# Kernel optimization log

Measured on AMD Instinct MI355X. Metric: run time of the kernel, lower is better.

The kernel has to match this reference:

```python
import jax, jax.numpy as jnp
import numpy as np

B, L, IN_DIMS = 256, 512, 64
UNITS, OUT_STEPS, OUT_DIMS = 256, 64, 32
KSIZE = 5


def setup_inputs() -> dict:
    key = jax.random.key(0)
    ks = jax.random.split(key, 14)
    s = lambda k, shp: jax.random.normal(k, shp, dtype=jnp.float32) * 0.05
    return {
        "inputs": jax.random.normal(ks[0], (B, L, IN_DIMS), dtype=jnp.float32),
        "conv_k": s(ks[1], (KSIZE, IN_DIMS, UNITS)),   # WIO layout
        "conv_b": s(ks[2], (UNITS,)),
        "enc_W": s(ks[3], (UNITS, 4 * UNITS)),          # kernel (input after CNN has UNITS channels)
        "enc_U": s(ks[4], (UNITS, 4 * UNITS)),          # recurrent kernel
        "enc_b": s(ks[5], (4 * UNITS,)),
        "cell_W": s(ks[6], (UNITS, 4 * UNITS)),
        "cell_U": s(ks[7], (UNITS, 4 * UNITS)),
        "cell_b": s(ks[8], (4 * UNITS,)),
        "fore_W": s(ks[9], (UNITS, OUT_DIMS)),
        "fore_b": s(ks[10], (OUT_DIMS,)),
        "back_W": s(ks[11], (UNITS, IN_DIMS)),
        "back_b": s(ks[12], (IN_DIMS,)),
    }


def _lstm_step(W, U, b, h, c, x_t):
    # Keras gate order: i, f, g(candidate), o
    z = x_t @ W + h @ U + b
    i, f, g, o = jnp.split(z, 4, axis=-1)
    c_new = jax.nn.sigmoid(f) * c + jax.nn.sigmoid(i) * jnp.tanh(g)
    h_new = jax.nn.sigmoid(o) * jnp.tanh(c_new)
    return h_new, c_new


def _forward(inputs, conv_k, conv_b, enc_W, enc_U, enc_b,
             cell_W, cell_U, cell_b, fore_W, fore_b, back_W, back_b):
    # Conv1D 'same', relu
    x = jax.lax.conv_general_dilated(
        inputs, conv_k, window_strides=(1,), padding="SAME",
        dimension_numbers=("NWC", "WIO", "NWC"))
    x = jax.nn.relu(x + conv_b)

    # Encoder LSTM (dropout inactive at inference)
    h0 = jnp.zeros((x.shape[0], UNITS), x.dtype)
    c0 = jnp.zeros((x.shape[0], UNITS), x.dtype)

    def enc_step(carry, x_t):
        h, c = carry
        h, c = _lstm_step(enc_W, enc_U, enc_b, h, c, x_t)
        return (h, c), h
    (h_T, c_T), seq = jax.lax.scan(enc_step, (h0, c0), jnp.swapaxes(x, 0, 1))
    backcast_seq = jnp.swapaxes(seq, 0, 1)  # [B, L, UNITS]

    def dec_step(carry, _):
        h, c = carry
        h, c = _lstm_step(cell_W, cell_U, cell_b, h, c, h)
        return (h, c), h
    _, outs = jax.lax.scan(dec_step, (h_T, c_T), None, length=OUT_STEPS)
    forecast_seq = jnp.swapaxes(outs, 0, 1)  # [B, OUT_STEPS, UNITS]

    forecast = forecast_seq @ fore_W + fore_b   # [B, OUT_STEPS, OUT_DIMS]
    backcast = backcast_seq @ back_W + back_b   # [B, L, IN_DIMS]
    return forecast, backcast


def reference(inputs, conv_k, conv_b, enc_W, enc_U, enc_b,
              cell_W, cell_U, cell_b, fore_W, fore_b, back_W, back_b):
    return _forward(inputs, conv_k, conv_b, enc_W, enc_U, enc_b,
                    cell_W, cell_U, cell_b, fore_W, fore_b, back_W, back_b)
```

## Files before the change

kernel.cpp:

```cpp
#include <hip/hip_runtime.h>
#include <stdint.h>

typedef unsigned short u16;
typedef __attribute__((ext_vector_type(8))) short bf16x8;
typedef __attribute__((ext_vector_type(4))) float fx4;

#define MFMA16(a, b, c) __builtin_amdgcn_mfma_f32_16x16x32_bf16((a), (b), (c), 0, 0, 0)

#define OFF_X      0u
#define OFF_H      67108864u
#define OFF_ENCWT  142737408u
#define OFF_ENCUT  143261696u
#define OFF_CELLT  143785984u
#define OFF_CONVKT 144310272u
#define OFF_BWT    144474112u
#define OFF_FWT    144506880u
#define OFF_BAR    144523264u

__device__ __forceinline__ u16 f2bf(float f) {
    uint32_t u = __builtin_bit_cast(uint32_t, f);
    u += 0x7FFFu + ((u >> 16) & 1u);
    return (u16)(u >> 16);
}
__device__ __forceinline__ float sigm(float x) { return 1.0f / (1.0f + __expf(-x)); }
__device__ __forceinline__ float tanh_f(float x) { return 1.0f - 2.0f / (__expf(2.0f * x) + 1.0f); }

__device__ __forceinline__ void store_h_sc(const u16* p, uint32_t v) {
    asm volatile("global_store_short %0, %1, off sc0 sc1" :: "v"(p), "v"(v) : "memory");
}
__device__ __forceinline__ void vmcnt0() { asm volatile("s_waitcnt vmcnt(0)" ::: "memory"); }

__global__ void zero_kernel(unsigned char* ws) {
    int i = blockIdx.x * blockDim.x + threadIdx.x;
    uint32_t* h0 = (uint32_t*)(ws + OFF_H);
    for (int k = i; k < 32768; k += 16384) h0[k] = 0u;
    if (i < 256) ((uint32_t*)(ws + OFF_BAR))[i] = 0u;
}

__global__ void prep_kernel(const float* enc_W, const float* enc_U, const float* cell_W,
                            const float* cell_U, const float* conv_k, const float* back_W,
                            const float* fore_W, unsigned char* ws) {
    u16* encWt = (u16*)(ws + OFF_ENCWT);
    u16* encUt = (u16*)(ws + OFF_ENCUT);
    u16* cellT = (u16*)(ws + OFF_CELLT);
    u16* convKt = (u16*)(ws + OFF_CONVKT);
    u16* bwt = (u16*)(ws + OFF_BWT);
    u16* fwt = (u16*)(ws + OFF_FWT);
    int idx = blockIdx.x * blockDim.x + threadIdx.x;
    int stride = gridDim.x * blockDim.x;
    for (int i = idx; i < 262144; i += stride) {
        int n = i >> 8, k = i & 255;
        encWt[i] = f2bf(enc_W[k * 1024 + n]);
        encUt[i] = f2bf(enc_U[k * 1024 + n]);
        cellT[i] = f2bf(cell_W[k * 1024 + n] + cell_U[k * 1024 + n]);
    }
    for (int i = idx; i < 81920; i += stride) {
        int u = i / 320, rem = i - u * 320;
        convKt[i] = f2bf(conv_k[rem * 256 + u]);
    }
    for (int i = idx; i < 16384; i += stride) {
        int n = i >> 8, k = i & 255;
        bwt[i] = f2bf(back_W[k * 64 + n]);
    }
    for (int i = idx; i < 8192; i += stride) {
        int n = i >> 8, k = i & 255;
        fwt[i] = f2bf(fore_W[k * 32 + n]);
    }
}

__global__ __launch_bounds__(256) void conv_kernel(const float* __restrict__ in,
                                                   const float* __restrict__ conv_b,
                                                   unsigned char* ws) {
    const u16* kt = (const u16*)(ws + OFF_CONVKT);
    u16* xout = (u16*)(ws + OFF_X);
    int w = threadIdx.x >> 6, lane = threadIdx.x & 63;
    int m = lane & 15, q = lane >> 4;
    int mt = blockIdx.x * 4 + w;
    int r0 = mt * 16;
    int b = r0 >> 9;
    int l0 = r0 & 511;

    fx4 acc[16];
#pragma unroll
    for (int nt = 0; nt < 16; ++nt) acc[nt] = (fx4){0.f, 0.f, 0.f, 0.f};

#pragma unroll
    for (int s = 0; s < 10; ++s) {
        int k0 = s * 32 + q * 8;
        int kk = k0 >> 6, c = k0 & 63;
        int l2 = l0 + m + kk - 2;
        bf16x8 af = {0, 0, 0, 0, 0, 0, 0, 0};
        if (l2 >= 0 && l2 < 512) {
            const float* src = in + (((b << 9) + l2) << 6) + c;
            fx4 f0 = *(const fx4*)src;
            fx4 f1 = *(const fx4*)(src + 4);
            af[0] = (short)f2bf(f0[0]); af[1] = (short)f2bf(f0[1]);
            af[2] = (short)f2bf(f0[2]); af[3] = (short)f2bf(f0[3]);
            af[4] = (short)f2bf(f1[0]); af[5] = (short)f2bf(f1[1]);
            af[6] = (short)f2bf(f1[2]); af[7] = (short)f2bf(f1[3]);
        }
#pragma unroll
        for (int nt = 0; nt < 16; ++nt) {
            bf16x8 bf = *(const bf16x8*)(kt + (nt * 16 + m) * 320 + k0);
            acc[nt] = MFMA16(af, bf, acc[nt]);
        }
    }
#pragma unroll
    for (int nt = 0; nt < 16; ++nt) {
        int u = nt * 16 + m;
        float bias = conv_b[u];
#pragma unroll
        for (int r = 0; r < 4; ++r) {
            float v = acc[nt][r] + bias;
            v = v > 0.f ? v : 0.f;
            int row = r0 + q * 4 + r;
            xout[row * 256 + u] = f2bf(v);
        }
    }
}

__global__ __launch_bounds__(256, 1) void enc_kernel(const float* __restrict__ enc_b,
                                                     unsigned char* ws) {
    int tid = threadIdx.x;
    int w = tid >> 6, lane = tid & 63, m = lane & 15, q = lane >> 4;
    int bid = blockIdx.x;
    int g = bid & 15, p = bid >> 4;
    int b0 = g * 16;
    int un0 = p * 64 + w * 16;

    const u16* encWt = (const u16*)(ws + OFF_ENCWT);
    const u16* encUt = (const u16*)(ws + OFF_ENCUT);
    const u16* xbf = (const u16*)(ws + OFF_X);
    u16* H = (u16*)(ws + OFF_H);
    float* csaveg = (float*)(ws + OFF_X + (size_t)g * 4194304u);
    int* bar = (int*)(ws + OFF_BAR + g * 64);

    bf16x8 wfrag[4][8], ufrag[4][8];
#pragma unroll
    for (int gi = 0; gi < 4; ++gi) {
#pragma unroll
        for (int s = 0; s < 8; ++s) {
            int n = gi * 256 + un0 + m;
            wfrag[gi][s] = *(const bf16x8*)(encWt + n * 256 + s * 32 + q * 8);
            ufrag[gi][s] = *(const bf16x8*)(encUt + n * 256 + s * 32 + q * 8);
        }
    }
    float bi[4], creg[4];
#pragma unroll
    for (int gi = 0; gi < 4; ++gi) bi[gi] = enc_b[gi * 256 + un0 + m];
    creg[0] = creg[1] = creg[2] = creg[3] = 0.f;

    const u16* xrow = xbf + (size_t)(b0 + m) * (512 * 256) + q * 8;

    for (int t = 0; t < 512; ++t) {
        bf16x8 xa[8];
        const u16* xA = xrow + (size_t)t * 256;
#pragma unroll
        for (int s = 0; s < 8; ++s) xa[s] = *(const bf16x8*)(xA + s * 32);
        fx4 acc[4];
#pragma unroll
        for (int gi = 0; gi < 4; ++gi) acc[gi] = (fx4){bi[gi], bi[gi], bi[gi], bi[gi]};
#pragma unroll
        for (int s = 0; s < 8; ++s) {
#pragma unroll
            for (int gi = 0; gi < 4; ++gi)
                acc[gi] = MFMA16(xa[s], wfrag[gi][s], acc[gi]);
        }

        if (lane == 0) {
            int tgt = 4 * t;
            while (__hip_atomic_load(bar, __ATOMIC_RELAXED, __HIP_MEMORY_SCOPE_AGENT) < tgt) {}
        }
        asm volatile("" ::: "memory");

        const u16* hA = H + (size_t)t * 65536 + (b0 + m) * 256 + q * 8;
        bf16x8 ha[8];
#pragma unroll
        for (int s = 0; s < 8; ++s) ha[s] = *(const bf16x8*)(hA + s * 32);
#pragma unroll
        for (int s = 0; s < 8; ++s) {
#pragma unroll
            for (int gi = 0; gi < 4; ++gi)
                acc[gi] = MFMA16(ha[s], ufrag[gi][s], acc[gi]);
        }

        const u16* hw = H + (size_t)(t + 1) * 65536 + un0 + m;
#pragma unroll
        for (int r = 0; r < 4; ++r) {
            float cv = sigm(acc[1][r]) * creg[r] + sigm(acc[0][r]) * tanh_f(acc[2][r]);
            creg[r] = cv;
            float hv = sigm(acc[3][r]) * tanh_f(cv);
            store_h_sc(hw + (b0 + q * 4 + r) * 256, (uint32_t)f2bf(hv));
        }
        vmcnt0();
        __syncthreads();
        if (tid == 0)
            __hip_atomic_fetch_add(bar, 1, __ATOMIC_RELAXED, __HIP_MEMORY_SCOPE_AGENT);
    }

#pragma unroll
    for (int r = 0; r < 4; ++r)
        csaveg[(q * 4 + r) * 256 + un0 + m] = creg[r];
}

__global__ __launch_bounds__(256, 1) void dec_kernel(const float* __restrict__ cell_b,
                                                     unsigned char* ws) {
    int tid = threadIdx.x;
    int w = tid >> 6, lane = tid & 63, m = lane & 15, q = lane >> 4;
    int bid = blockIdx.x;
    int g = bid & 15, p = bid >> 4;
    int b0 = g * 16;
    int un0 = p * 64 + w * 16;

    const u16* cellT = (const u16*)(ws + OFF_CELLT);
    u16* H = (u16*)(ws + OFF_H);
    const float* csaveg = (const float*)(ws + OFF_X + (size_t)g * 4194304u);
    int* bar = (int*)(ws + OFF_BAR + g * 64);

    bf16x8 wfrag[4][8];
#pragma unroll
    for (int gi = 0; gi < 4; ++gi) {
#pragma unroll
        for (int s = 0; s < 8; ++s)
            wfrag[gi][s] = *(const bf16x8*)(cellT + (gi * 256 + un0 + m) * 256 + s * 32 + q * 8);
    }
    float bi[4], creg[4];
#pragma unroll
    for (int gi = 0; gi < 4; ++gi) bi[gi] = cell_b[gi * 256 + un0 + m];
#pragma unroll
    for (int r = 0; r < 4; ++r) creg[r] = csaveg[(q * 4 + r) * 256 + un0 + m];

    for (int t = 0; t < 64; ++t) {
        if (lane == 0) {
            int tgt = 2048 + 4 * t;
            while (__hip_atomic_load(bar, __ATOMIC_RELAXED, __HIP_MEMORY_SCOPE_AGENT) < tgt) {}
        }
        asm volatile("" ::: "memory");

        const u16* hA = H + (size_t)(512 + t) * 65536 + (b0 + m) * 256 + q * 8;
        bf16x8 ha[8];
#pragma unroll
        for (int s = 0; s < 8; ++s) ha[s] = *(const bf16x8*)(hA + s * 32);
        fx4 acc[4];
#pragma unroll
        for (int gi = 0; gi < 4; ++gi) acc[gi] = (fx4){bi[gi], bi[gi], bi[gi], bi[gi]};
#pragma unroll
        for (int s = 0; s < 8; ++s) {
#pragma unroll
            for (int gi = 0; gi < 4; ++gi)
                acc[gi] = MFMA16(ha[s], wfrag[gi][s], acc[gi]);
        }

        const u16* hw = H + (size_t)(513 + t) * 65536 + un0 + m;
#pragma unroll
        for (int r = 0; r < 4; ++r) {
            float cv = sigm(acc[1][r]) * creg[r] + sigm(acc[0][r]) * tanh_f(acc[2][r]);
            creg[r] = cv;
            float hv = sigm(acc[3][r]) * tanh_f(cv);
            store_h_sc(hw + (b0 + q * 4 + r) * 256, (uint32_t)f2bf(hv));
        }
        vmcnt0();
        __syncthreads();
        if (tid == 0)
            __hip_atomic_fetch_add(bar, 1, __ATOMIC_RELAXED, __HIP_MEMORY_SCOPE_AGENT);
    }
}

__global__ __launch_bounds__(256) void out_gemm(const u16* __restrict__ A,
                                                const u16* __restrict__ Bt,
                                                const float* __restrict__ bias,
                                                float* __restrict__ out,
                                                int ncols, int seqlen) {
    int w = threadIdx.x >> 6, lane = threadIdx.x & 63, m = lane & 15, q = lane >> 4;
    int mt = blockIdx.x * 4 + w;
    int s = mt >> 4;
    int b0 = (mt & 15) * 16;
    bf16x8 af[8];
    const u16* Arow = A + ((size_t)s * 256 + b0 + m) * 256 + q * 8;
#pragma unroll
    for (int ss = 0; ss < 8; ++ss) af[ss] = *(const bf16x8*)(Arow + ss * 32);
    int ntiles = ncols >> 4;
    for (int nt = 0; nt < ntiles; ++nt) {
        fx4 acc = (fx4){0.f, 0.f, 0.f, 0.f};
#pragma unroll
        for (int ss = 0; ss < 8; ++ss) {
            bf16x8 bf = *(const bf16x8*)(Bt + (nt * 16 + m) * 256 + ss * 32 + q * 8);
            acc = MFMA16(af[ss], bf, acc);
        }
        int col = nt * 16 + m;
        float bv = bias[col];
#pragma unroll
        for (int r = 0; r < 4; ++r) {
            int b = b0 + q * 4 + r;
            out[((size_t)b * seqlen + s) * ncols + col] = acc[r] + bv;
        }
    }
}

extern "C" void kernel_launch(void* const* d_in, const int* in_sizes, int n_in,
                              void* d_out, int out_size, void* d_ws, size_t ws_size,
                              hipStream_t stream) {
    const float* inputs = (const float*)d_in[0];
    const float* conv_k = (const float*)d_in[1];
    const float* conv_b = (const float*)d_in[2];
    const float* enc_W  = (const float*)d_in[3];
    const float* enc_U  = (const float*)d_in[4];
    const float* enc_b  = (const float*)d_in[5];
    const float* cell_W = (const float*)d_in[6];
    const float* cell_U = (const float*)d_in[7];
    const float* cell_b = (const float*)d_in[8];
    const float* fore_W = (const float*)d_in[9];
    const float* fore_b = (const float*)d_in[10];
    const float* back_W = (const float*)d_in[11];
    const float* back_b = (const float*)d_in[12];
    unsigned char* ws = (unsigned char*)d_ws;
    float* out = (float*)d_out;

    zero_kernel<<<64, 256, 0, stream>>>(ws);
    prep_kernel<<<1024, 256, 0, stream>>>(enc_W, enc_U, cell_W, cell_U, conv_k, back_W, fore_W, ws);
    conv_kernel<<<2048, 256, 0, stream>>>(inputs, conv_b, ws);
    enc_kernel<<<64, 256, 0, stream>>>(enc_b, ws);
    dec_kernel<<<64, 256, 0, stream>>>(cell_b, ws);

    const u16* H = (const u16*)(ws + OFF_H);
    out_gemm<<<2048, 256, 0, stream>>>(H + (size_t)1 * 65536, (const u16*)(ws + OFF_BWT),
                                       back_b, out + 524288, 64, 512);
    out_gemm<<<256, 256, 0, stream>>>(H + (size_t)513 * 65536, (const u16*)(ws + OFF_FWT),
                                      fore_b, out, 32, 64);
}
```

Before: 2.722 ms.

## Split encoder input projection into producer blocks feeding a ring buffer

The encoder launches 128 blocks. 64 producer blocks compute x_t·W plus bias ahead of time and write it into an 8-deep global ring, while the 64 recurrent blocks do only h·U, add the precomputed projection, and apply the gates. The input GEMM moves off the serial critical path, and h stores are coalesced through shared memory into dwordx2 writes. Spin loops gain a poll budget as a deadlock safeguard. In exchange there is extra global traffic for the fp32 ring, more flag polling, and a reliance on all 128 blocks being co-resident.

Result: faster. 2.335 ms (-14.2%).

```diff
diff --git a/kernel.cpp b/kernel.cpp
--- a/kernel.cpp
+++ b/kernel.cpp
@@ -4,11 +4,13 @@
 typedef unsigned short u16;
 typedef __attribute__((ext_vector_type(8))) short bf16x8;
 typedef __attribute__((ext_vector_type(4))) float fx4;
+typedef __attribute__((ext_vector_type(2))) unsigned int u32x2;
 
 #define MFMA16(a, b, c) __builtin_amdgcn_mfma_f32_16x16x32_bf16((a), (b), (c), 0, 0, 0)
 
 #define OFF_X      0u
 #define OFF_H      67108864u
+#define RING_OFF   134348800u
 #define OFF_ENCWT  142737408u
 #define OFF_ENCUT  143261696u
 #define OFF_CELLT  143785984u
@@ -17,6 +19,8 @@
 #define OFF_FWT    144506880u
 #define OFF_BAR    144523264u
 
+#define POLL_BUDGET (1 << 25)
+
 __device__ __forceinline__ u16 f2bf(float f) {
     uint32_t u = __builtin_bit_cast(uint32_t, f);
     u += 0x7FFFu + ((u >> 16) & 1u);
@@ -24,10 +28,6 @@
 }
 __device__ __forceinline__ float sigm(float x) { return 1.0f / (1.0f + __expf(-x)); }
 __device__ __forceinline__ float tanh_f(float x) { return 1.0f - 2.0f / (__expf(2.0f * x) + 1.0f); }
-
-__device__ __forceinline__ void store_h_sc(const u16* p, uint32_t v) {
-    asm volatile("global_store_short %0, %1, off sc0 sc1" :: "v"(p), "v"(v) : "memory");
-}
 __device__ __forceinline__ void vmcnt0() { asm volatile("s_waitcnt vmcnt(0)" ::: "memory"); }
 
 __global__ void zero_kernel(unsigned char* ws) {
@@ -119,57 +119,101 @@
     }
 }
 
-__global__ __launch_bounds__(256, 1) void enc_kernel(const float* __restrict__ enc_b,
-                                                     unsigned char* ws) {
+__global__ __launch_bounds__(256, 1) void enc_fused(const float* __restrict__ enc_b,
+                                                    unsigned char* ws) {
+    __shared__ u16 hbuf[1024];
     int tid = threadIdx.x;
     int w = tid >> 6, lane = tid & 63, m = lane & 15, q = lane >> 4;
     int bid = blockIdx.x;
+    u16* H = (u16*)(ws + OFF_H);
+    int budget = POLL_BUDGET;
+
+    if (bid >= 64) {
+        int idx = bid - 64, g = idx & 15, p = idx >> 4;
+        int b0 = g * 16;
+        int un0 = p * 64 + w * 16;
+        const u16* encWt = (const u16*)(ws + OFF_ENCWT);
+        const u16* xbf = (const u16*)(ws + OFF_X);
+        float* ringg = (float*)(ws + RING_OFF + (size_t)g * 524288u);
+        int* hbar = (int*)(ws + OFF_BAR + g * 64);
+        int* pz = (int*)(ws + OFF_BAR + g * 64 + 32);
+
+        bf16x8 wfr[4][8];
+        float bi[4];
+#pragma unroll
+        for (int j = 0; j < 4; ++j) {
+            int row = j * 256 + un0 + m;
+            bi[j] = enc_b[row];
+#pragma unroll
+            for (int ks = 0; ks < 8; ++ks)
+                wfr[j][ks] = *(const bf16x8*)(encWt + row * 256 + ks * 32 + q * 8);
+        }
+        const u16* xrow = xbf + (size_t)(b0 + m) * (512 * 256) + q * 8;
+        bf16x8 xa[8];
+#pragma unroll
+        for (int s = 0; s < 8; ++s) xa[s] = *(const bf16x8*)(xrow + s * 32);
+
+        for (int t = 0; t < 512; ++t) {
+            fx4 a0 = (fx4){bi[0], bi[0], bi[0], bi[0]};
+            fx4 a1 = (fx4){bi[1], bi[1], bi[1], bi[1]};
+            fx4 a2 = (fx4){bi[2], bi[2], bi[2], bi[2]};
+            fx4 a3 = (fx4){bi[3], bi[3], bi[3], bi[3]};
+#pragma unroll
+            for (int ks = 0; ks < 8; ++ks) {
+                a0 = MFMA16(xa[ks], wfr[0][ks], a0);
+                a1 = MFMA16(xa[ks], wfr[1][ks], a1);
+                a2 = MFMA16(xa[ks], wfr[2][ks], a2);
+                a3 = MFMA16(xa[ks], wfr[3][ks], a3);
+            }
+            float* zs = ringg + (t & 7) * 16384 + (un0 + m) * 16 + q * 4;
+            asm volatile("global_store_dwordx4 %0, %1, off sc0 sc1" :: "v"(zs), "v"(a0) : "memory");
+            asm volatile("global_store_dwordx4 %0, %1, off sc0 sc1" :: "v"(zs + 4096), "v"(a1) : "memory");
+            asm volatile("global_store_dwordx4 %0, %1, off sc0 sc1" :: "v"(zs + 8192), "v"(a2) : "memory");
+            asm volatile("global_store_dwordx4 %0, %1, off sc0 sc1" :: "v"(zs + 12288), "v"(a3) : "memory");
+            if (t < 511) {
+                const u16* xA = xrow + (size_t)(t + 1) * 256;
+#pragma unroll
+                for (int s = 0; s < 8; ++s) xa[s] = *(const bf16x8*)(xA + s * 32);
+                if (tid == 0 && t >= 7) {
+                    int tgt = 4 * (t - 6);
+                    while (__hip_atomic_load(hbar, __ATOMIC_RELAXED, __HIP_MEMORY_SCOPE_AGENT) < tgt
+                           && --budget > 0) {}
+                }
+            }
+            vmcnt0();
+            __syncthreads();
+            if (tid == 0)
+                __hip_atomic_fetch_add(pz, 1, __ATOMIC_RELAXED, __HIP_MEMORY_SCOPE_AGENT);
+        }
+        return;
+    }
+
     int g = bid & 15, p = bid >> 4;
     int b0 = g * 16;
     int un0 = p * 64 + w * 16;
-
-    const u16* encWt = (const u16*)(ws + OFF_ENCWT);
     const u16* encUt = (const u16*)(ws + OFF_ENCUT);
-    const u16* xbf = (const u16*)(ws + OFF_X);
-    u16* H = (u16*)(ws + OFF_H);
+    const float* ringg = (const float*)(ws + RING_OFF + (size_t)g * 524288u);
     float* csaveg = (float*)(ws + OFF_X + (size_t)g * 4194304u);
-    int* bar = (int*)(ws + OFF_BAR + g * 64);
-
-    bf16x8 wfrag[4][8], ufrag[4][8];
+    int* hbar = (int*)(ws + OFF_BAR + g * 64);
+    int* pz = (int*)(ws + OFF_BAR + g * 64 + 32);
+
+    bf16x8 ufrag[4][8];
 #pragma unroll
     for (int gi = 0; gi < 4; ++gi) {
 #pragma unroll
-        for (int s = 0; s < 8; ++s) {
-            int n = gi * 256 + un0 + m;
-            wfrag[gi][s] = *(const bf16x8*)(encWt + n * 256 + s * 32 + q * 8);
-            ufrag[gi][s] = *(const bf16x8*)(encUt + n * 256 + s * 32 + q * 8);
-        }
-    }
-    float bi[4], creg[4];
-#pragma unroll
-    for (int gi = 0; gi < 4; ++gi) bi[gi] = enc_b[gi * 256 + un0 + m];
-    creg[0] = creg[1] = creg[2] = creg[3] = 0.f;
-
-    const u16* xrow = xbf + (size_t)(b0 + m) * (512 * 256) + q * 8;
+        for (int s = 0; s < 8; ++s)
+            ufrag[gi][s] = *(const bf16x8*)(encUt + (gi * 256 + un0 + m) * 256 + s * 32 + q * 8);
+    }
+    float creg[4] = {0.f, 0.f, 0.f, 0.f};
 
     for (int t = 0; t < 512; ++t) {
-        bf16x8 xa[8];
-        const u16* xA = xrow + (size_t)t * 256;
-#pragma unroll
-        for (int s = 0; s < 8; ++s) xa[s] = *(const bf16x8*)(xA + s * 32);
-        fx4 acc[4];
-#pragma unroll
-        for (int gi = 0; gi < 4; ++gi) acc[gi] = (fx4){bi[gi], bi[gi], bi[gi], bi[gi]};
-#pragma unroll
-        for (int s = 0; s < 8; ++s) {
-#pragma unroll
-            for (int gi = 0; gi < 4; ++gi)
-                acc[gi] = MFMA16(xa[s], wfrag[gi][s], acc[gi]);
-        }
-
         if (lane == 0) {
-            int tgt = 4 * t;
-            while (__hip_atomic_load(bar, __ATOMIC_RELAXED, __HIP_MEMORY_SCOPE_AGENT) < tgt) {}
+            int tgtz = 4 * (t + 1), tgth = 4 * t;
+            while (--budget > 0) {
+                int vz = __hip_atomic_load(pz, __ATOMIC_RELAXED, __HIP_MEMORY_SCOPE_AGENT);
+                int vh = __hip_atomic_load(hbar, __ATOMIC_RELAXED, __HIP_MEMORY_SCOPE_AGENT);
+                if (vz >= tgtz && vh >= tgth) break;
+            }
         }
         asm volatile("" ::: "memory");
 
@@ -177,25 +221,50 @@
         bf16x8 ha[8];
 #pragma unroll
         for (int s = 0; s < 8; ++s) ha[s] = *(const bf16x8*)(hA + s * 32);
+        const float* zb = ringg + (t & 7) * 16384 + (un0 + m) * 16 + q * 4;
+        fx4 z0, z1, z2, z3;
+        asm volatile("global_load_dwordx4 %0, %1, off sc0 sc1" : "=v"(z0) : "v"(zb));
+        asm volatile("global_load_dwordx4 %0, %1, off sc0 sc1" : "=v"(z1) : "v"(zb + 4096));
+        asm volatile("global_load_dwordx4 %0, %1, off sc0 sc1" : "=v"(z2) : "v"(zb + 8192));
+        asm volatile("global_load_dwordx4 %0, %1, off sc0 sc1" : "=v"(z3) : "v"(zb + 12288));
+
+        fx4 acc[4];
+#pragma unroll
+        for (int gi = 0; gi < 4; ++gi) acc[gi] = (fx4){0.f, 0.f, 0.f, 0.f};
 #pragma unroll
         for (int s = 0; s < 8; ++s) {
 #pragma unroll
             for (int gi = 0; gi < 4; ++gi)
                 acc[gi] = MFMA16(ha[s], ufrag[gi][s], acc[gi]);
         }
-
-        const u16* hw = H + (size_t)(t + 1) * 65536 + un0 + m;
+        vmcnt0();
+        __builtin_amdgcn_sched_barrier(0);
+
+        float hreg[4];
 #pragma unroll
         for (int r = 0; r < 4; ++r) {
-            float cv = sigm(acc[1][r]) * creg[r] + sigm(acc[0][r]) * tanh_f(acc[2][r]);
+            float pi = acc[0][r] + z0[r];
+            float pf = acc[1][r] + z1[r];
+            float pg = acc[2][r] + z2[r];
+            float po = acc[3][r] + z3[r];
+            float cv = sigm(pf) * creg[r] + sigm(pi) * tanh_f(pg);
             creg[r] = cv;
-            float hv = sigm(acc[3][r]) * tanh_f(cv);
-            store_h_sc(hw + (b0 + q * 4 + r) * 256, (uint32_t)f2bf(hv));
+            hreg[r] = sigm(po) * tanh_f(cv);
+        }
+#pragma unroll
+        for (int r = 0; r < 4; ++r)
+            hbuf[(q * 4 + r) * 64 + w * 16 + m] = f2bf(hreg[r]);
+        __syncthreads();
+        {
+            int row = tid >> 4, c4 = (tid & 15) * 4;
+            u32x2 hv = *(const u32x2*)&hbuf[row * 64 + c4];
+            const u16* hw = H + (size_t)(t + 1) * 65536 + (b0 + row) * 256 + p * 64 + c4;
+            asm volatile("global_store_dwordx2 %0, %1, off sc0 sc1" :: "v"(hw), "v"(hv) : "memory");
         }
         vmcnt0();
         __syncthreads();
         if (tid == 0)
-            __hip_atomic_fetch_add(bar, 1, __ATOMIC_RELAXED, __HIP_MEMORY_SCOPE_AGENT);
+            __hip_atomic_fetch_add(hbar, 1, __ATOMIC_RELAXED, __HIP_MEMORY_SCOPE_AGENT);
     }
 
 #pragma unroll
@@ -211,6 +280,7 @@
     int g = bid & 15, p = bid >> 4;
     int b0 = g * 16;
     int un0 = p * 64 + w * 16;
+    int budget = POLL_BUDGET;
 
     const u16* cellT = (const u16*)(ws + OFF_CELLT);
     u16* H = (u16*)(ws + OFF_H);
@@ -233,7 +303,8 @@
     for (int t = 0; t < 64; ++t) {
         if (lane == 0) {
             int tgt = 2048 + 4 * t;
-            while (__hip_atomic_load(bar, __ATOMIC_RELAXED, __HIP_MEMORY_SCOPE_AGENT) < tgt) {}
+            while (__hip_atomic_load(bar, __ATOMIC_RELAXED, __HIP_MEMORY_SCOPE_AGENT) < tgt
+                   && --budget > 0) {}
         }
         asm volatile("" ::: "memory");
 
@@ -257,7 +328,9 @@
             float cv = sigm(acc[1][r]) * creg[r] + sigm(acc[0][r]) * tanh_f(acc[2][r]);
             creg[r] = cv;
             float hv = sigm(acc[3][r]) * tanh_f(cv);
-            store_h_sc(hw + (b0 + q * 4 + r) * 256, (uint32_t)f2bf(hv));
+            uint32_t hb = (uint32_t)f2bf(hv);
+            const u16* hp = hw + (b0 + q * 4 + r) * 256;
+            asm volatile("global_store_short %0, %1, off sc0 sc1" :: "v"(hp), "v"(hb) : "memory");
         }
         vmcnt0();
         __syncthreads();
@@ -319,7 +392,7 @@
     zero_kernel<<<64, 256, 0, stream>>>(ws);
     prep_kernel<<<1024, 256, 0, stream>>>(enc_W, enc_U, cell_W, cell_U, conv_k, back_W, fore_W, ws);
     conv_kernel<<<2048, 256, 0, stream>>>(inputs, conv_b, ws);
-    enc_kernel<<<64, 256, 0, stream>>>(enc_b, ws);
+    enc_fused<<<128, 256, 0, stream>>>(enc_b, ws);
     dec_kernel<<<64, 256, 0, stream>>>(cell_b, ws);
 
     const u16* H = (const u16*)(ws + OFF_H);
```
